# Kernel tuning notes

Hardware: AMD Instinct MI355X
Metric: run time of the kernel (lower is better)

## Reference

```python
import jax, jax.numpy as jnp
import numpy as np

N = 100000   # nodes
E = 600000   # edges
B = 512      # graphs in batch
H = 128      # hidden dim
ED = 8       # edge feature dim
TWO48 = float(2 ** 48 - 1)


def _w(k, shape, fan_in):
    return jax.random.normal(k, shape, jnp.float32) * (1.0 / np.sqrt(fan_in))


def setup_inputs() -> dict:
    key = jax.random.key(0)
    ks = jax.random.split(key, 32)
    inp = {}
    inp["s_node_ids"] = jax.random.randint(ks[0], (N,), 0, 2 ** 31 - 1, dtype=jnp.int32)
    inp["s_edge_index"] = jax.random.randint(ks[1], (2, E), 0, N, dtype=jnp.int32)
    inp["s_edge_attr"] = jax.random.normal(ks[2], (E, ED), jnp.float32)
    inp["s_batch"] = jnp.sort(jax.random.randint(ks[3], (N,), 0, B, dtype=jnp.int32))
    inp["depth"] = jax.random.uniform(ks[4], (B,), jnp.float32)
    # id_mlp: Linear(1,H) -> ReLU -> Linear(H,H)
    inp["id_w1"] = _w(ks[5], (1, H), 1); inp["id_b1"] = jnp.zeros((H,), jnp.float32)
    inp["id_w2"] = _w(ks[6], (H, H), H); inp["id_b2"] = jnp.zeros((H,), jnp.float32)
    # edge_mlp: Linear(ED,H) -> ReLU -> Linear(H,H)
    inp["ed_w1"] = _w(ks[7], (ED, H), ED); inp["ed_b1"] = jnp.zeros((H,), jnp.float32)
    inp["ed_w2"] = _w(ks[8], (H, H), H); inp["ed_b2"] = jnp.zeros((H,), jnp.float32)
    # GINEConv nn MLPs: Linear(H,H) -> ReLU -> Linear(H,H)
    inp["c1_w1"] = _w(ks[9], (H, H), H); inp["c1_b1"] = jnp.zeros((H,), jnp.float32)
    inp["c1_w2"] = _w(ks[10], (H, H), H); inp["c1_b2"] = jnp.zeros((H,), jnp.float32)
    inp["c2_w1"] = _w(ks[11], (H, H), H); inp["c2_b1"] = jnp.zeros((H,), jnp.float32)
    inp["c2_w2"] = _w(ks[12], (H, H), H); inp["c2_b2"] = jnp.zeros((H,), jnp.float32)
    inp["rg_w1"] = _w(ks[13], (H + 1, H), H + 1); inp["rg_b1"] = jnp.zeros((H,), jnp.float32)
    inp["rg_w2"] = _w(ks[14], (H, 1), H); inp["rg_b2"] = jnp.zeros((1,), jnp.float32)
    return inp


def _mlp2(x, w1, b1, w2, b2):
    return jax.nn.relu(x @ w1 + b1) @ w2 + b2


def _gine(x, src, dst, e, w1, b1, w2, b2):
    # message = ReLU(x_j + e), sum-aggregated at dst; out = nn((1+eps)*x + aggr), eps=0
    msg = jax.nn.relu(x[src] + e)                       # [E, H]
    aggr = jax.ops.segment_sum(msg, dst, num_segments=N)  # [N, H]
    return _mlp2(x + aggr, w1, b1, w2, b2)


def _global_mean(x, batch):
    sums = jax.ops.segment_sum(x, batch, num_segments=B)                          # [B, H]
    cnts = jax.ops.segment_sum(jnp.ones((x.shape[0], 1), x.dtype), batch, num_segments=B)
    return sums / jnp.maximum(cnts, 1.0)


def reference(s_node_ids, s_edge_index, s_edge_attr, s_batch, depth,
              id_w1, id_b1, id_w2, id_b2,
              ed_w1, ed_b1, ed_w2, ed_b2,
              c1_w1, c1_b1, c1_w2, c1_b2,
              c2_w1, c2_b1, c2_w2, c2_b2,
              rg_w1, rg_b1, rg_w2, rg_b2):
    src, dst = s_edge_index[0], s_edge_index[1]
    x0 = jnp.clip(s_node_ids.astype(jnp.float32) / TWO48, 0.0, 1.0)[:, None]  # [N,1]
    x = _mlp2(x0, id_w1, id_b1, id_w2, id_b2)                                 # [N,H]
    e = _mlp2(s_edge_attr, ed_w1, ed_b1, ed_w2, ed_b2)                        # [E,H]
    x = jax.nn.relu(_gine(x, src, dst, e, c1_w1, c1_b1, c1_w2, c1_b2))
    x = jax.nn.relu(_gine(x, src, dst, e, c2_w1, c2_b1, c2_w2, c2_b2))
    rep = jnp.concatenate([_global_mean(x, s_batch), depth[:, None]], axis=1)  # [B,H+1]
    return _mlp2(rep, rg_w1, rg_b1, rg_w2, rg_b2)[:, 0]                        # [B]
```

## Files before the change

### kernel.cpp

```cpp
#include <hip/hip_runtime.h>
#include <hip/hip_bf16.h>

#define N_NODES 100000
#define N_EDGES 600000
#define NB      512
#define H       128
#define ED      8
#define SCAN_CHUNK 1024
#define N_CHUNKS   98

typedef __attribute__((ext_vector_type(8))) short short8;
typedef __attribute__((ext_vector_type(4))) float f32x4;
typedef __attribute__((ext_vector_type(4))) unsigned int u32x4;
typedef unsigned short u16;
typedef unsigned int   u32;

static __device__ __forceinline__ u16 f2bf(float f) {
    u32 u = __float_as_uint(f);
    u32 r = u + 0x7fffu + ((u >> 16) & 1u);
    return (u16)(r >> 16);
}
static __device__ __forceinline__ float bf2f(u32 h) {
    return __uint_as_float(h << 16);
}

__global__ __launch_bounds__(256) void pack_all_kernel(
    const float* __restrict__ W0, const float* __restrict__ W1,
    const float* __restrict__ W2, const float* __restrict__ W3,
    const float* __restrict__ W4, const float* __restrict__ W5,
    const float* __restrict__ W6,
    short8* __restrict__ O0, short8* __restrict__ O1,
    short8* __restrict__ O2, short8* __restrict__ O3,
    short8* __restrict__ O4, short8* __restrict__ O5,
    short8* __restrict__ O6)
{
    int gid = blockIdx.x * 256 + threadIdx.x;
    const int total = 512 + 6 * 2048;
    if (gid >= total) return;
    const float* W; short8* O; int Krows, kkmax, slot;
    if (gid < 512) { W = W0; O = O0; Krows = ED; kkmax = 1; slot = gid; }
    else {
        int m = (gid - 512) / 2048;
        slot = (gid - 512) % 2048;
        Krows = H; kkmax = 4;
        switch (m) {
            case 0: W = W1; O = O1; break;
            case 1: W = W2; O = O2; break;
            case 2: W = W3; O = O3; break;
            case 3: W = W4; O = O4; break;
            case 4: W = W5; O = O5; break;
            default: W = W6; O = O6; break;
        }
    }
    int lane = slot & 63;
    int t = slot >> 6;
    int nt = t & 1; t >>= 1;
    int kk = t % kkmax;
    int w  = t / kkmax;
    int quad = lane >> 4, n15 = lane & 15;
    int n = w * 32 + nt * 16 + n15;
    short8 v;
    #pragma unroll
    for (int j = 0; j < 8; j++) {
        int k = kk * 32 + quad * 8 + j;
        v[j] = (k < Krows) ? (short)f2bf(W[k * H + n]) : (short)0;
    }
    O[slot] = v;
}

__global__ __launch_bounds__(256) void hist_kernel(
    const int* __restrict__ edge_index, int* __restrict__ counts)
{
    int e = blockIdx.x * 256 + threadIdx.x;
    if (e < N_EDGES) atomicAdd(&counts[edge_index[N_EDGES + e]], 1);
}

__global__ __launch_bounds__(SCAN_CHUNK) void scan1_kernel(
    const int* __restrict__ counts, int* __restrict__ chunk_scan,
    int* __restrict__ bsum_raw)
{
    __shared__ int s[SCAN_CHUNK];
    int tid = threadIdx.x;
    int gid = blockIdx.x * SCAN_CHUNK + tid;
    int v = counts[gid];
    s[tid] = v;
    __syncthreads();
    #pragma unroll
    for (int off = 1; off < SCAN_CHUNK; off <<= 1) {
        int t = (tid >= off) ? s[tid - off] : 0;
        __syncthreads();
        s[tid] += t;
        __syncthreads();
    }
    chunk_scan[gid] = s[tid] - v;
    if (tid == SCAN_CHUNK - 1) bsum_raw[blockIdx.x] = s[tid];
}

__global__ __launch_bounds__(128) void scan2_kernel(
    const int* __restrict__ bsum_raw, int* __restrict__ bsum_scan)
{
    __shared__ int s[128];
    int tid = threadIdx.x;
    int v = (tid < N_CHUNKS) ? bsum_raw[tid] : 0;
    s[tid] = v;
    __syncthreads();
    #pragma unroll
    for (int off = 1; off < 128; off <<= 1) {
        int t = (tid >= off) ? s[tid - off] : 0;
        __syncthreads();
        s[tid] += t;
        __syncthreads();
    }
    bsum_scan[tid] = s[tid] - v;
}

__global__ __launch_bounds__(256) void fill_kernel(
    const int* __restrict__ edge_index,
    const int* __restrict__ chunk_scan, const int* __restrict__ bsum_scan,
    int* __restrict__ counts, int* __restrict__ src_list,
    int* __restrict__ pos_of)
{
    int e = blockIdx.x * 256 + threadIdx.x;
    if (e >= N_EDGES) return;
    int src = edge_index[e];
    int dst = edge_index[N_EDGES + e];
    int slot = atomicAdd(&counts[dst], -1) - 1;
    int pos = chunk_scan[dst] + bsum_scan[dst >> 10] + slot;
    src_list[pos] = src;
    pos_of[e] = pos;
}

__global__ __launch_bounds__(256) void finalize_offsets(
    const int* __restrict__ chunk_scan, const int* __restrict__ bsum_scan,
    int* __restrict__ row_start)
{
    int i = blockIdx.x * 256 + threadIdx.x;
    if (i <= N_NODES) row_start[i] = chunk_scan[i] + bsum_scan[i >> 10];
}

__global__ __launch_bounds__(256) void node_mlp_mfma(
    const int* __restrict__ ids,
    const float* __restrict__ w1, const float* __restrict__ b1,
    const short8* __restrict__ pW2, const float* __restrict__ b2,
    u16* __restrict__ x_out)
{
    __shared__ u16 sH[64 * 136];
    __shared__ float s_x0[64];
    int tid = threadIdx.x;
    int w = tid >> 6, lane = tid & 63, quad = lane >> 4, n15 = lane & 15;
    short8 fW2[4][2];
    #pragma unroll
    for (int kk = 0; kk < 4; kk++) {
        fW2[kk][0] = pW2[((w * 4 + kk) * 2 + 0) * 64 + lane];
        fW2[kk][1] = pW2[((w * 4 + kk) * 2 + 1) * 64 + lane];
    }
    float rb2[2] = { b2[w * 32 + n15], b2[w * 32 + 16 + n15] };
    float w1c = w1[tid & 127], b1c = b1[tid & 127];
    const int ntile = (N_NODES + 63) / 64;
    for (int tile = blockIdx.x; tile < ntile; tile += gridDim.x) {
        int row0 = tile * 64;
        if (tid < 64) {
            int n = row0 + tid;
            float x0 = (n < N_NODES) ? (float)ids[n] / 281474976710655.0f : 0.0f;
            s_x0[tid] = fminf(fmaxf(x0, 0.0f), 1.0f);
        }
        __syncthreads();
        int half = tid >> 7, c = tid & 127;
        #pragma unroll 8
        for (int rr = 0; rr < 32; rr++) {
            int r = half + rr * 2;
            sH[r * 136 + c] = f2bf(fmaxf(s_x0[r] * w1c + b1c, 0.0f));
        }
        __syncthreads();
        f32x4 acc[4][2];
        #pragma unroll
        for (int s = 0; s < 4; s++) { acc[s][0] = (f32x4){0,0,0,0}; acc[s][1] = (f32x4){0,0,0,0}; }
        #pragma unroll
        for (int kk = 0; kk < 4; kk++) {
            #pragma unroll
            for (int s = 0; s < 4; s++) {
                short8 a = *(const short8*)&sH[(s * 16 + n15) * 136 + kk * 32 + quad * 8];
                acc[s][0] = __builtin_amdgcn_mfma_f32_16x16x32_bf16(a, fW2[kk][0], acc[s][0], 0, 0, 0);
                acc[s][1] = __builtin_amdgcn_mfma_f32_16x16x32_bf16(a, fW2[kk][1], acc[s][1], 0, 0, 0);
            }
        }
        __syncthreads();
        #pragma unroll
        for (int s = 0; s < 4; s++)
            #pragma unroll
            for (int nt = 0; nt < 2; nt++) {
                int col = w * 32 + nt * 16 + n15;
                #pragma unroll
                for (int reg = 0; reg < 4; reg++)
                    sH[(s * 16 + quad * 4 + reg) * 136 + col] =
                        f2bf(acc[s][nt][reg] + rb2[nt]);
            }
        __syncthreads();
        for (int idx = tid; idx < 64 * 16; idx += 256) {
            int r = idx >> 4, c8 = (idx & 15) << 3;
            int n = row0 + r;
            if (n < N_NODES)
                *(uint4*)&x_out[(long)n * H + c8] = *(const uint4*)&sH[r * 136 + c8];
        }
        __syncthreads();
    }
}

__global__ __launch_bounds__(256) void edge_mlp_mfma(
    const float* __restrict__ attr,
    const int* __restrict__ pos_of,
    const short8* __restrict__ pW1, const float* __restrict__ b1,
    const short8* __restrict__ pW2, const float* __restrict__ b2,
    u16* __restrict__ e_perm)
{
    __shared__ u16 sA[64 * 40];
    __shared__ u16 sH[64 * 136];
    __shared__ int sPos[64];
    int tid = threadIdx.x;
    int w = tid >> 6, lane = tid & 63, quad = lane >> 4, n15 = lane & 15;
    short8 fW1[2];
    fW1[0] = pW1[(w * 2 + 0) * 64 + lane];
    fW1[1] = pW1[(w * 2 + 1) * 64 + lane];
    short8 fW2[4][2];
    #pragma unroll
    for (int kk = 0; kk < 4; kk++) {
        fW2[kk][0] = pW2[((w * 4 + kk) * 2 + 0) * 64 + lane];
        fW2[kk][1] = pW2[((w * 4 + kk) * 2 + 1) * 64 + lane];
    }
    float rb1[2] = { b1[w * 32 + n15], b1[w * 32 + 16 + n15] };
    float rb2[2] = { b2[w * 32 + n15], b2[w * 32 + 16 + n15] };
    const int ntile = N_EDGES / 64;
    for (int tile = blockIdx.x; tile < ntile; tile += gridDim.x) {
        int row0 = tile * 64;
        if (tid < 64) sPos[tid] = pos_of[row0 + tid];
        if (tid >= 64 && tid < 192) {
            int t2 = tid - 64;
            int r = t2 >> 1, c4 = (t2 & 1) * 4;
            f32x4 v = __builtin_nontemporal_load((const f32x4*)&attr[(long)(row0 + r) * ED + c4]);
            ushort4 o;
            o.x = f2bf(v[0]); o.y = f2bf(v[1]); o.z = f2bf(v[2]); o.w = f2bf(v[3]);
            *(ushort4*)&sA[r * 40 + c4] = o;
        } else if (tid >= 192) {
            int idx = tid - 192;
            for (; idx < 192; idx += 64) {
                int r = idx / 3, c8 = 8 + (idx % 3) * 8;
                *(uint4*)&sA[r * 40 + c8] = make_uint4(0, 0, 0, 0);
            }
        }
        __syncthreads();
        f32x4 acc[4][2];
        #pragma unroll
        for (int s = 0; s < 4; s++) { acc[s][0] = (f32x4){0,0,0,0}; acc[s][1] = (f32x4){0,0,0,0}; }
        #pragma unroll
        for (int s = 0; s < 4; s++) {
            short8 a = *(const short8*)&sA[(s * 16 + n15) * 40 + quad * 8];
            acc[s][0] = __builtin_amdgcn_mfma_f32_16x16x32_bf16(a, fW1[0], acc[s][0], 0, 0, 0);
            acc[s][1] = __builtin_amdgcn_mfma_f32_16x16x32_bf16(a, fW1[1], acc[s][1], 0, 0, 0);
        }
        #pragma unroll
        for (int s = 0; s < 4; s++)
            #pragma unroll
            for (int nt = 0; nt < 2; nt++) {
                int col = w * 32 + nt * 16 + n15;
                #pragma unroll
                for (int reg = 0; reg < 4; reg++)
                    sH[(s * 16 + quad * 4 + reg) * 136 + col] =
                        f2bf(fmaxf(acc[s][nt][reg] + rb1[nt], 0.0f));
            }
        __syncthreads();
        #pragma unroll
        for (int s = 0; s < 4; s++) { acc[s][0] = (f32x4){0,0,0,0}; acc[s][1] = (f32x4){0,0,0,0}; }
        #pragma unroll
        for (int kk = 0; kk < 4; kk++) {
            #pragma unroll
            for (int s = 0; s < 4; s++) {
                short8 a = *(const short8*)&sH[(s * 16 + n15) * 136 + kk * 32 + quad * 8];
                acc[s][0] = __builtin_amdgcn_mfma_f32_16x16x32_bf16(a, fW2[kk][0], acc[s][0], 0, 0, 0);
                acc[s][1] = __builtin_amdgcn_mfma_f32_16x16x32_bf16(a, fW2[kk][1], acc[s][1], 0, 0, 0);
            }
        }
        __syncthreads();
        #pragma unroll
        for (int s = 0; s < 4; s++)
            #pragma unroll
            for (int nt = 0; nt < 2; nt++) {
                int col = w * 32 + nt * 16 + n15;
                #pragma unroll
                for (int reg = 0; reg < 4; reg++)
                    sH[(s * 16 + quad * 4 + reg) * 136 + col] =
                        f2bf(acc[s][nt][reg] + rb2[nt]);
            }
        __syncthreads();
        for (int idx = tid; idx < 64 * 16; idx += 256) {
            int r = idx >> 4, c8 = (idx & 15) << 3;
            long rr = sPos[r];
            u32x4 v = *(const u32x4*)&sH[r * 136 + c8];
            __builtin_nontemporal_store(v, (u32x4*)&e_perm[rr * H + c8]);
        }
        __syncthreads();
    }
}

static __device__ __forceinline__ void acc8(float* a, u32x4 xv, u32x4 ev) {
    #pragma unroll
    for (int q = 0; q < 4; q++) {
        a[2 * q + 0] += fmaxf(bf2f(xv[q] & 0xffff) + bf2f(ev[q] & 0xffff), 0.0f);
        a[2 * q + 1] += fmaxf(bf2f(xv[q] >> 16)    + bf2f(ev[q] >> 16),    0.0f);
    }
}

__global__ __launch_bounds__(256) void aggregate_kernel(
    const int* __restrict__ row_start,
    const int* __restrict__ src_list,
    const u16* __restrict__ e_perm,
    const u16* __restrict__ x,
    u16* __restrict__ xs_out)
{
    int tid  = threadIdx.x;
    int lane = tid & 63;
    int l16  = lane & 15;
    int base = lane & 48;
    int fo   = l16 * 8;
    int n = blockIdx.x * 16 + (tid >> 4);
    const u16* xb = x + fo;

    int beg = row_start[n];
    int end = row_start[n + 1];
    float a[8], b[8];
    #pragma unroll
    for (int q = 0; q < 8; q++) { a[q] = 0.0f; b[q] = 0.0f; }

    for (int j0 = beg; j0 < end; j0 += 16) {
        int m = min(16, end - j0);
        int sv = src_list[j0 + min(l16, m - 1)];
        const u16* ej = e_perm + (long)j0 * H + fo;
        int j = 0;
        for (; j + 2 <= m; j += 2) {
            int s0 = __shfl(sv, base | j);
            int s1 = __shfl(sv, base | (j + 1));
            u32x4 xv0 = *(const u32x4*)(xb + (long)s0 * H);
            u32x4 ev0 = __builtin_nontemporal_load((const u32x4*)(ej + (long)(j + 0) * H));
            u32x4 xv1 = *(const u32x4*)(xb + (long)s1 * H);
            u32x4 ev1 = __builtin_nontemporal_load((const u32x4*)(ej + (long)(j + 1) * H));
            acc8(a, xv0, ev0);
            acc8(b, xv1, ev1);
        }
        if (j < m) {
            int s0 = __shfl(sv, base | j);
            u32x4 xv0 = *(const u32x4*)(xb + (long)s0 * H);
            u32x4 ev0 = __builtin_nontemporal_load((const u32x4*)(ej + (long)j * H));
            acc8(a, xv0, ev0);
        }
    }
    u32x4 xself = *(const u32x4*)(xb + (long)n * H);
    u32x4 out;
    #pragma unroll
    for (int q = 0; q < 4; q++) {
        float o0 = bf2f(xself[q] & 0xffff) + a[2 * q + 0] + b[2 * q + 0];
        float o1 = bf2f(xself[q] >> 16)    + a[2 * q + 1] + b[2 * q + 1];
        out[q] = (u32)f2bf(o0) | ((u32)f2bf(o1) << 16);
    }
    __builtin_nontemporal_store(out, (u32x4*)&xs_out[(long)n * H + fo]);
}

__global__ __launch_bounds__(256) void conv_mlp_mfma(
    const u16* __restrict__ xs,
    const short8* __restrict__ pW1, const float* __restrict__ b1,
    const short8* __restrict__ pW2, const float* __restrict__ b2,
    u16* __restrict__ x_out)
{
    __shared__ u16 sA[32 * 136];
    int tid = threadIdx.x;
    int w = tid >> 6, lane = tid & 63, quad = lane >> 4, n15 = lane & 15;
    short8 fW1[4][2], fW2[4][2];
    #pragma unroll
    for (int kk = 0; kk < 4; kk++) {
        fW1[kk][0] = pW1[((w * 4 + kk) * 2 + 0) * 64 + lane];
        fW1[kk][1] = pW1[((w * 4 + kk) * 2 + 1) * 64 + lane];
        fW2[kk][0] = pW2[((w * 4 + kk) * 2 + 0) * 64 + lane];
        fW2[kk][1] = pW2[((w * 4 + kk) * 2 + 1) * 64 + lane];
    }
    float rb1[2] = { b1[w * 32 + n15], b1[w * 32 + 16 + n15] };
    float rb2[2] = { b2[w * 32 + n15], b2[w * 32 + 16 + n15] };
    const int ntile = N_NODES / 32;
    for (int tile = blockIdx.x; tile < ntile; tile += gridDim.x) {
        long row0 = (long)tile * 32;
        for (int idx = tid; idx < 32 * 16; idx += 256) {
            int r = idx >> 4, c8 = (idx & 15) << 3;
            *(uint4*)&sA[r * 136 + c8] = *(const uint4*)&xs[(row0 + r) * H + c8];
        }
        __syncthreads();
        f32x4 acc[2][2];
        #pragma unroll
        for (int s = 0; s < 2; s++) { acc[s][0] = (f32x4){0,0,0,0}; acc[s][1] = (f32x4){0,0,0,0}; }
        #pragma unroll
        for (int kk = 0; kk < 4; kk++) {
            #pragma unroll
            for (int s = 0; s < 2; s++) {
                short8 a = *(const short8*)&sA[(s * 16 + n15) * 136 + kk * 32 + quad * 8];
                acc[s][0] = __builtin_amdgcn_mfma_f32_16x16x32_bf16(a, fW1[kk][0], acc[s][0], 0, 0, 0);
                acc[s][1] = __builtin_amdgcn_mfma_f32_16x16x32_bf16(a, fW1[kk][1], acc[s][1], 0, 0, 0);
            }
        }
        __syncthreads();
        #pragma unroll
        for (int s = 0; s < 2; s++)
            #pragma unroll
            for (int nt = 0; nt < 2; nt++) {
                int col = w * 32 + nt * 16 + n15;
                #pragma unroll
                for (int reg = 0; reg < 4; reg++)
                    sA[(s * 16 + quad * 4 + reg) * 136 + col] =
                        f2bf(fmaxf(acc[s][nt][reg] + rb1[nt], 0.0f));
            }
        __syncthreads();
        #pragma unroll
        for (int s = 0; s < 2; s++) { acc[s][0] = (f32x4){0,0,0,0}; acc[s][1] = (f32x4){0,0,0,0}; }
        #pragma unroll
        for (int kk = 0; kk < 4; kk++) {
            #pragma unroll
            for (int s = 0; s < 2; s++) {
                short8 a = *(const short8*)&sA[(s * 16 + n15) * 136 + kk * 32 + quad * 8];
                acc[s][0] = __builtin_amdgcn_mfma_f32_16x16x32_bf16(a, fW2[kk][0], acc[s][0], 0, 0, 0);
                acc[s][1] = __builtin_amdgcn_mfma_f32_16x16x32_bf16(a, fW2[kk][1], acc[s][1], 0, 0, 0);
            }
        }
        __syncthreads();
        #pragma unroll
        for (int s = 0; s < 2; s++)
            #pragma unroll
            for (int nt = 0; nt < 2; nt++) {
                int col = w * 32 + nt * 16 + n15;
                #pragma unroll
                for (int reg = 0; reg < 4; reg++)
                    sA[(s * 16 + quad * 4 + reg) * 136 + col] =
                        f2bf(fmaxf(acc[s][nt][reg] + rb2[nt], 0.0f));
            }
        __syncthreads();
        for (int idx = tid; idx < 32 * 16; idx += 256) {
            int r = idx >> 4, c8 = (idx & 15) << 3;
            *(uint4*)&x_out[(row0 + r) * H + c8] = *(const uint4*)&sA[r * 136 + c8];
        }
        __syncthreads();
    }
}

__global__ __launch_bounds__(256) void pool_kernel(
    const u16* __restrict__ x, const int* __restrict__ batch,
    float* __restrict__ sums, float* __restrict__ cnt)
{
    int sg   = threadIdx.x >> 6;
    int lane = threadIdx.x & 63;
    int fo = lane * 2;
    const int nper = (N_NODES + gridDim.x - 1) / gridDim.x;
    int n0 = blockIdx.x * nper;
    int n1 = min(n0 + nper, N_NODES);
    int cur = -1;
    float a0 = 0.0f, a1 = 0.0f, c = 0.0f;
    for (int n = n0 + sg; n < n1; n += 4) {
        int b = batch[n];
        if (b != cur) {
            if (cur >= 0) {
                atomicAdd(&sums[cur * H + fo],     a0);
                atomicAdd(&sums[cur * H + fo + 1], a1);
                if (lane == 0) atomicAdd(&cnt[cur], c);
            }
            a0 = a1 = 0.0f; c = 0.0f; cur = b;
        }
        u32 xv = *(const u32*)&x[(long)n * H + fo];
        a0 += bf2f(xv & 0xffff);
        a1 += bf2f(xv >> 16);
        c += 1.0f;
    }
    if (cur >= 0) {
        atomicAdd(&sums[cur * H + fo],     a0);
        atomicAdd(&sums[cur * H + fo + 1], a1);
        if (lane == 0) atomicAdd(&cnt[cur], c);
    }
}

__global__ __launch_bounds__(128) void regressor_kernel(
    const float* __restrict__ sums, const float* __restrict__ cnt,
    const float* __restrict__ depth,
    const float* __restrict__ w1, const float* __restrict__ b1,
    const float* __restrict__ w2, const float* __restrict__ b2,
    float* __restrict__ out)
{
    __shared__ float s_mean[H];
    __shared__ float s_red[2];
    int b = blockIdx.x;
    int j = threadIdx.x;
    float c = fmaxf(cnt[b], 1.0f);
    s_mean[j] = sums[b * H + j] / c;
    __syncthreads();
    float h = b1[j];
    #pragma unroll 8
    for (int k = 0; k < H; k++) h += s_mean[k] * w1[k * H + j];
    h += depth[b] * w1[H * H + j];
    h = fmaxf(h, 0.0f);
    float p = h * w2[j];
    #pragma unroll
    for (int off = 32; off >= 1; off >>= 1) p += __shfl_down(p, off, 64);
    if ((j & 63) == 0) s_red[j >> 6] = p;
    __syncthreads();
    if (j == 0) out[b] = s_red[0] + s_red[1] + b2[0];
}

extern "C" void kernel_launch(void* const* d_in, const int* in_sizes, int n_in,
                              void* d_out, int out_size, void* d_ws, size_t ws_size,
                              hipStream_t stream)
{
    const int*   ids   = (const int*)  d_in[0];
    const int*   eidx  = (const int*)  d_in[1];
    const float* eattr = (const float*)d_in[2];
    const int*   batch = (const int*)  d_in[3];
    const float* depth = (const float*)d_in[4];
    const float* id_w1 = (const float*)d_in[5];
    const float* id_b1 = (const float*)d_in[6];
    const float* id_w2 = (const float*)d_in[7];
    const float* id_b2 = (const float*)d_in[8];
    const float* ed_w1 = (const float*)d_in[9];
    const float* ed_b1 = (const float*)d_in[10];
    const float* ed_w2 = (const float*)d_in[11];
    const float* ed_b2 = (const float*)d_in[12];
    const float* c1_w1 = (const float*)d_in[13];
    const float* c1_b1 = (const float*)d_in[14];
    const float* c1_w2 = (const float*)d_in[15];
    const float* c1_b2 = (const float*)d_in[16];
    const float* c2_w1 = (const float*)d_in[17];
    const float* c2_b1 = (const float*)d_in[18];
    const float* c2_w2 = (const float*)d_in[19];
    const float* c2_b2 = (const float*)d_in[20];
    const float* rg_w1 = (const float*)d_in[21];
    const float* rg_b1 = (const float*)d_in[22];
    const float* rg_w2 = (const float*)d_in[23];
    const float* rg_b2 = (const float*)d_in[24];

    char* ws = (char*)d_ws;
    u16*   e_buf    = (u16*)  (ws);
    u16*   x_buf    = (u16*)  (ws + 153600000);
    u16*   xs_buf   = (u16*)  (ws + 179200000);
    float* sums_buf = (float*)(ws + 204800000);
    float* cnt_buf  = (float*)(ws + 205062144);
    int*   counts   = (int*)  (ws + 205064192);
    int*   chunk_sc = (int*)  (ws + 205465600);
    int*   bsum_raw = (int*)  (ws + 205867008);
    int*   bsum_sc  = (int*)  (ws + 205867520);
    int*   src_list = (int*)  (ws + 205868032);
    int*   pos_of   = (int*)  (ws + 208268032);
    short8* ed_w1p  = (short8*)(ws + 210668032);
    short8* ed_w2p  = (short8*)(ws + 210676224);
    short8* c1_w1p  = (short8*)(ws + 210708992);
    short8* c1_w2p  = (short8*)(ws + 210741760);
    short8* c2_w1p  = (short8*)(ws + 210774528);
    short8* c2_w2p  = (short8*)(ws + 210807296);
    short8* id_w2p  = (short8*)(ws + 210840064);
    int*   row_start = counts;

    pack_all_kernel<<<50, 256, 0, stream>>>(
        ed_w1, ed_w2, c1_w1, c1_w2, c2_w1, c2_w2, id_w2,
        ed_w1p, ed_w2p, c1_w1p, c1_w2p, c2_w1p, c2_w2p, id_w2p);

    hipMemsetAsync(counts, 0, 401408, stream);
    hist_kernel <<<(N_EDGES + 255) / 256, 256, 0, stream>>>(eidx, counts);
    scan1_kernel<<<N_CHUNKS, SCAN_CHUNK, 0, stream>>>(counts, chunk_sc, bsum_raw);
    scan2_kernel<<<1, 128, 0, stream>>>(bsum_raw, bsum_sc);
    fill_kernel <<<(N_EDGES + 255) / 256, 256, 0, stream>>>(eidx, chunk_sc, bsum_sc,
                                                            counts, src_list, pos_of);
    finalize_offsets<<<(N_NODES + 256) / 256, 256, 0, stream>>>(chunk_sc, bsum_sc, row_start);

    node_mlp_mfma<<<768, 256, 0, stream>>>(ids, id_w1, id_b1, id_w2p, id_b2, x_buf);
    edge_mlp_mfma<<<2048, 256, 0, stream>>>(eattr, pos_of, ed_w1p, ed_b1, ed_w2p, ed_b2, e_buf);

    aggregate_kernel<<<6250, 256, 0, stream>>>(row_start, src_list, e_buf, x_buf, xs_buf);
    conv_mlp_mfma<<<3125, 256, 0, stream>>>(xs_buf, c1_w1p, c1_b1, c1_w2p, c1_b2, x_buf);

    aggregate_kernel<<<6250, 256, 0, stream>>>(row_start, src_list, e_buf, x_buf, xs_buf);
    conv_mlp_mfma<<<3125, 256, 0, stream>>>(xs_buf, c2_w1p, c2_b1, c2_w2p, c2_b2, x_buf);

    hipMemsetAsync(sums_buf, 0, (size_t)(NB * H + NB) * 4, stream);
    pool_kernel<<<2048, 256, 0, stream>>>(x_buf, batch, sums_buf, cnt_buf);
    regressor_kernel<<<NB, 128, 0, stream>>>(sums_buf, cnt_buf, depth,
                                             rg_w1, rg_b1, rg_w2, rg_b2, (float*)d_out);
}
```

Measured before the change: 408.1 us.

## Permute edge attributes in fill, pack bf16 pairs, aggregate two nodes per group

The fill kernel now converts edge attributes to bf16 and scatters them into CSR order. The edge MLP can then read its inputs directly into registers and write the edge embeddings contiguously, with no pos_of indirection, no scattered stores and no LDS staging of the input. Bf16 rounding now uses the packed v_cvt_pk_bf16_f32 instruction across all MLP epilogues. The aggregate kernel handles two destination nodes per 16-lane group with interleaved loads to raise memory-level parallelism, at the cost of more registers, more complex control flow and half as many blocks.

```diff
diff --git a/kernel.cpp b/kernel.cpp
--- a/kernel.cpp
+++ b/kernel.cpp
@@ -22,6 +22,11 @@
 }
 static __device__ __forceinline__ float bf2f(u32 h) {
     return __uint_as_float(h << 16);
+}
+static __device__ __forceinline__ u32 bfpack(float lo, float hi) {
+    u32 r;
+    asm("v_cvt_pk_bf16_f32 %0, %1, %2" : "=v"(r) : "v"(lo), "v"(hi));
+    return r;
 }
 
 __global__ __launch_bounds__(256) void pack_all_kernel(
@@ -118,7 +123,7 @@
     const int* __restrict__ edge_index,
     const int* __restrict__ chunk_scan, const int* __restrict__ bsum_scan,
     int* __restrict__ counts, int* __restrict__ src_list,
-    int* __restrict__ pos_of)
+    const float* __restrict__ attr, u16* __restrict__ attr_perm)
 {
     int e = blockIdx.x * 256 + threadIdx.x;
     if (e >= N_EDGES) return;
@@ -127,7 +132,13 @@
     int slot = atomicAdd(&counts[dst], -1) - 1;
     int pos = chunk_scan[dst] + bsum_scan[dst >> 10] + slot;
     src_list[pos] = src;
-    pos_of[e] = pos;
+    float4 v0 = *(const float4*)&attr[(long)e * ED];
+    float4 v1 = *(const float4*)&attr[(long)e * ED + 4];
+    u32 w0 = bfpack(v0.x, v0.y);
+    u32 w1 = bfpack(v0.z, v0.w);
+    u32 w2 = bfpack(v1.x, v1.y);
+    u32 w3 = bfpack(v1.z, v1.w);
+    *(uint4*)&attr_perm[(long)pos * ED] = make_uint4(w0, w1, w2, w3);
 }
 
 __global__ __launch_bounds__(256) void finalize_offsets(
@@ -166,10 +177,13 @@
         }
         __syncthreads();
         int half = tid >> 7, c = tid & 127;
-        #pragma unroll 8
-        for (int rr = 0; rr < 32; rr++) {
+        #pragma unroll
+        for (int rr = 0; rr < 32; rr += 2) {
             int r = half + rr * 2;
-            sH[r * 136 + c] = f2bf(fmaxf(s_x0[r] * w1c + b1c, 0.0f));
+            u32 p = bfpack(fmaxf(s_x0[r] * w1c + b1c, 0.0f),
+                           fmaxf(s_x0[r + 2] * w1c + b1c, 0.0f));
+            sH[r * 136 + c]       = (u16)p;
+            sH[(r + 2) * 136 + c] = (u16)(p >> 16);
         }
         __syncthreads();
         f32x4 acc[4][2];
@@ -190,10 +204,13 @@
             #pragma unroll
             for (int nt = 0; nt < 2; nt++) {
                 int col = w * 32 + nt * 16 + n15;
-                #pragma unroll
-                for (int reg = 0; reg < 4; reg++)
-                    sH[(s * 16 + quad * 4 + reg) * 136 + col] =
-                        f2bf(acc[s][nt][reg] + rb2[nt]);
+                int rb = (s * 16 + quad * 4) * 136 + col;
+                u32 p0 = bfpack(acc[s][nt][0] + rb2[nt], acc[s][nt][1] + rb2[nt]);
+                u32 p1 = bfpack(acc[s][nt][2] + rb2[nt], acc[s][nt][3] + rb2[nt]);
+                sH[rb]       = (u16)p0;
+                sH[rb + 136] = (u16)(p0 >> 16);
+                sH[rb + 272] = (u16)p1;
+                sH[rb + 408] = (u16)(p1 >> 16);
             }
         __syncthreads();
         for (int idx = tid; idx < 64 * 16; idx += 256) {
@@ -207,15 +224,12 @@
 }
 
 __global__ __launch_bounds__(256) void edge_mlp_mfma(
-    const float* __restrict__ attr,
-    const int* __restrict__ pos_of,
+    const u16* __restrict__ attr_perm,
     const short8* __restrict__ pW1, const float* __restrict__ b1,
     const short8* __restrict__ pW2, const float* __restrict__ b2,
     u16* __restrict__ e_perm)
 {
-    __shared__ u16 sA[64 * 40];
     __shared__ u16 sH[64 * 136];
-    __shared__ int sPos[64];
     int tid = threadIdx.x;
     int w = tid >> 6, lane = tid & 63, quad = lane >> 4, n15 = lane & 15;
     short8 fW1[2];
@@ -229,43 +243,39 @@
     }
     float rb1[2] = { b1[w * 32 + n15], b1[w * 32 + 16 + n15] };
     float rb2[2] = { b2[w * 32 + n15], b2[w * 32 + 16 + n15] };
+    const short8 zero8 = (short8){0,0,0,0,0,0,0,0};
     const int ntile = N_EDGES / 64;
     for (int tile = blockIdx.x; tile < ntile; tile += gridDim.x) {
         int row0 = tile * 64;
-        if (tid < 64) sPos[tid] = pos_of[row0 + tid];
-        if (tid >= 64 && tid < 192) {
-            int t2 = tid - 64;
-            int r = t2 >> 1, c4 = (t2 & 1) * 4;
-            f32x4 v = __builtin_nontemporal_load((const f32x4*)&attr[(long)(row0 + r) * ED + c4]);
-            ushort4 o;
-            o.x = f2bf(v[0]); o.y = f2bf(v[1]); o.z = f2bf(v[2]); o.w = f2bf(v[3]);
-            *(ushort4*)&sA[r * 40 + c4] = o;
-        } else if (tid >= 192) {
-            int idx = tid - 192;
-            for (; idx < 192; idx += 64) {
-                int r = idx / 3, c8 = 8 + (idx % 3) * 8;
-                *(uint4*)&sA[r * 40 + c8] = make_uint4(0, 0, 0, 0);
-            }
-        }
-        __syncthreads();
+        short8 av[4];
+        #pragma unroll
+        for (int s = 0; s < 4; s++) {
+            av[s] = zero8;
+            if (quad == 0)
+                av[s] = *(const short8*)&attr_perm[(long)(row0 + s * 16 + n15) * ED];
+        }
         f32x4 acc[4][2];
         #pragma unroll
         for (int s = 0; s < 4; s++) { acc[s][0] = (f32x4){0,0,0,0}; acc[s][1] = (f32x4){0,0,0,0}; }
         #pragma unroll
         for (int s = 0; s < 4; s++) {
-            short8 a = *(const short8*)&sA[(s * 16 + n15) * 40 + quad * 8];
-            acc[s][0] = __builtin_amdgcn_mfma_f32_16x16x32_bf16(a, fW1[0], acc[s][0], 0, 0, 0);
-            acc[s][1] = __builtin_amdgcn_mfma_f32_16x16x32_bf16(a, fW1[1], acc[s][1], 0, 0, 0);
+            acc[s][0] = __builtin_amdgcn_mfma_f32_16x16x32_bf16(av[s], fW1[0], acc[s][0], 0, 0, 0);
+            acc[s][1] = __builtin_amdgcn_mfma_f32_16x16x32_bf16(av[s], fW1[1], acc[s][1], 0, 0, 0);
         }
         #pragma unroll
         for (int s = 0; s < 4; s++)
             #pragma unroll
             for (int nt = 0; nt < 2; nt++) {
                 int col = w * 32 + nt * 16 + n15;
-                #pragma unroll
-                for (int reg = 0; reg < 4; reg++)
-                    sH[(s * 16 + quad * 4 + reg) * 136 + col] =
-                        f2bf(fmaxf(acc[s][nt][reg] + rb1[nt], 0.0f));
+                int rb = (s * 16 + quad * 4) * 136 + col;
+                u32 p0 = bfpack(fmaxf(acc[s][nt][0] + rb1[nt], 0.0f),
+                                fmaxf(acc[s][nt][1] + rb1[nt], 0.0f));
+                u32 p1 = bfpack(fmaxf(acc[s][nt][2] + rb1[nt], 0.0f),
+                                fmaxf(acc[s][nt][3] + rb1[nt], 0.0f));
+                sH[rb]       = (u16)p0;
+                sH[rb + 136] = (u16)(p0 >> 16);
+                sH[rb + 272] = (u16)p1;
+                sH[rb + 408] = (u16)(p1 >> 16);
             }
         __syncthreads();
         #pragma unroll
@@ -285,17 +295,18 @@
             #pragma unroll
             for (int nt = 0; nt < 2; nt++) {
                 int col = w * 32 + nt * 16 + n15;
-                #pragma unroll
-                for (int reg = 0; reg < 4; reg++)
-                    sH[(s * 16 + quad * 4 + reg) * 136 + col] =
-                        f2bf(acc[s][nt][reg] + rb2[nt]);
+                int rb = (s * 16 + quad * 4) * 136 + col;
+                u32 p0 = bfpack(acc[s][nt][0] + rb2[nt], acc[s][nt][1] + rb2[nt]);
+                u32 p1 = bfpack(acc[s][nt][2] + rb2[nt], acc[s][nt][3] + rb2[nt]);
+                sH[rb]       = (u16)p0;
+                sH[rb + 136] = (u16)(p0 >> 16);
+                sH[rb + 272] = (u16)p1;
+                sH[rb + 408] = (u16)(p1 >> 16);
             }
         __syncthreads();
         for (int idx = tid; idx < 64 * 16; idx += 256) {
             int r = idx >> 4, c8 = (idx & 15) << 3;
-            long rr = sPos[r];
-            u32x4 v = *(const u32x4*)&sH[r * 136 + c8];
-            __builtin_nontemporal_store(v, (u32x4*)&e_perm[rr * H + c8]);
+            *(uint4*)&e_perm[(long)(row0 + r) * H + c8] = *(const uint4*)&sH[r * 136 + c8];
         }
         __syncthreads();
     }
@@ -321,46 +332,111 @@
     int l16  = lane & 15;
     int base = lane & 48;
     int fo   = l16 * 8;
-    int n = blockIdx.x * 16 + (tid >> 4);
+    int g    = tid >> 4;
+    int nA   = blockIdx.x * 32 + g * 2;
     const u16* xb = x + fo;
 
-    int beg = row_start[n];
-    int end = row_start[n + 1];
-    float a[8], b[8];
-    #pragma unroll
-    for (int q = 0; q < 8; q++) { a[q] = 0.0f; b[q] = 0.0f; }
-
-    for (int j0 = beg; j0 < end; j0 += 16) {
-        int m = min(16, end - j0);
-        int sv = src_list[j0 + min(l16, m - 1)];
-        const u16* ej = e_perm + (long)j0 * H + fo;
-        int j = 0;
-        for (; j + 2 <= m; j += 2) {
-            int s0 = __shfl(sv, base | j);
-            int s1 = __shfl(sv, base | (j + 1));
-            u32x4 xv0 = *(const u32x4*)(xb + (long)s0 * H);
-            u32x4 ev0 = __builtin_nontemporal_load((const u32x4*)(ej + (long)(j + 0) * H));
-            u32x4 xv1 = *(const u32x4*)(xb + (long)s1 * H);
-            u32x4 ev1 = __builtin_nontemporal_load((const u32x4*)(ej + (long)(j + 1) * H));
-            acc8(a, xv0, ev0);
-            acc8(b, xv1, ev1);
-        }
-        if (j < m) {
-            int s0 = __shfl(sv, base | j);
-            u32x4 xv0 = *(const u32x4*)(xb + (long)s0 * H);
-            u32x4 ev0 = __builtin_nontemporal_load((const u32x4*)(ej + (long)j * H));
-            acc8(a, xv0, ev0);
-        }
-    }
-    u32x4 xself = *(const u32x4*)(xb + (long)n * H);
-    u32x4 out;
+    int rsA = row_start[nA];
+    int rsB = row_start[nA + 1];
+    int rsC = row_start[nA + 2];
+    float a0[8], a1[8], b0[8], b1[8];
+    #pragma unroll
+    for (int q = 0; q < 8; q++) { a0[q] = 0.0f; a1[q] = 0.0f; b0[q] = 0.0f; b1[q] = 0.0f; }
+
+    int jA = rsA, endA = rsB;
+    int jB = rsB, endB = rsC;
+    while (jA < endA || jB < endB) {
+        int mA = endA - jA; mA = mA > 16 ? 16 : (mA < 0 ? 0 : mA);
+        int mB = endB - jB; mB = mB > 16 ? 16 : (mB < 0 ? 0 : mB);
+        int svA = mA ? src_list[jA + min(l16, mA - 1)] : 0;
+        int svB = mB ? src_list[jB + min(l16, mB - 1)] : 0;
+        const u16* eA = e_perm + (long)jA * H + fo;
+        const u16* eB = e_perm + (long)jB * H + fo;
+        int mD = mA < mB ? mA : mB;
+        int i = 0;
+        for (; i + 2 <= mD; i += 2) {
+            int sa0 = __shfl(svA, base | i);
+            int sa1 = __shfl(svA, base | (i + 1));
+            int sb0 = __shfl(svB, base | i);
+            int sb1 = __shfl(svB, base | (i + 1));
+            u32x4 va0 = *(const u32x4*)(xb + (long)sa0 * H);
+            u32x4 wa0 = *(const u32x4*)(eA + (long)(i + 0) * H);
+            u32x4 vb0 = *(const u32x4*)(xb + (long)sb0 * H);
+            u32x4 wb0 = *(const u32x4*)(eB + (long)(i + 0) * H);
+            u32x4 va1 = *(const u32x4*)(xb + (long)sa1 * H);
+            u32x4 wa1 = *(const u32x4*)(eA + (long)(i + 1) * H);
+            u32x4 vb1 = *(const u32x4*)(xb + (long)sb1 * H);
+            u32x4 wb1 = *(const u32x4*)(eB + (long)(i + 1) * H);
+            acc8(a0, va0, wa0);
+            acc8(b0, vb0, wb0);
+            acc8(a1, va1, wa1);
+            acc8(b1, vb1, wb1);
+        }
+        if (i < mD) {
+            int sa0 = __shfl(svA, base | i);
+            int sb0 = __shfl(svB, base | i);
+            u32x4 va0 = *(const u32x4*)(xb + (long)sa0 * H);
+            u32x4 wa0 = *(const u32x4*)(eA + (long)i * H);
+            u32x4 vb0 = *(const u32x4*)(xb + (long)sb0 * H);
+            u32x4 wb0 = *(const u32x4*)(eB + (long)i * H);
+            acc8(a0, va0, wa0);
+            acc8(b0, vb0, wb0);
+            i++;
+        }
+        int k = i;
+        for (; k + 2 <= mA; k += 2) {
+            int sa0 = __shfl(svA, base | k);
+            int sa1 = __shfl(svA, base | (k + 1));
+            u32x4 va0 = *(const u32x4*)(xb + (long)sa0 * H);
+            u32x4 wa0 = *(const u32x4*)(eA + (long)(k + 0) * H);
+            u32x4 va1 = *(const u32x4*)(xb + (long)sa1 * H);
+            u32x4 wa1 = *(const u32x4*)(eA + (long)(k + 1) * H);
+            acc8(a0, va0, wa0);
+            acc8(a1, va1, wa1);
+        }
+        if (k < mA) {
+            int sa0 = __shfl(svA, base | k);
+            u32x4 va0 = *(const u32x4*)(xb + (long)sa0 * H);
+            u32x4 wa0 = *(const u32x4*)(eA + (long)k * H);
+            acc8(a0, va0, wa0);
+        }
+        k = i;
+        for (; k + 2 <= mB; k += 2) {
+            int sb0 = __shfl(svB, base | k);
+            int sb1 = __shfl(svB, base | (k + 1));
+            u32x4 vb0 = *(const u32x4*)(xb + (long)sb0 * H);
+            u32x4 wb0 = *(const u32x4*)(eB + (long)(k + 0) * H);
+            u32x4 vb1 = *(const u32x4*)(xb + (long)sb1 * H);
+            u32x4 wb1 = *(const u32x4*)(eB + (long)(k + 1) * H);
+            acc8(b0, vb0, wb0);
+            acc8(b1, vb1, wb1);
+        }
+        if (k < mB) {
+            int sb0 = __shfl(svB, base | k);
+            u32x4 vb0 = *(const u32x4*)(xb + (long)sb0 * H);
+            u32x4 wb0 = *(const u32x4*)(eB + (long)k * H);
+            acc8(b0, vb0, wb0);
+        }
+        jA += mA; jB += mB;
+    }
+    u32x4 xvA = *(const u32x4*)(xb + (long)nA * H);
+    u32x4 oA;
     #pragma unroll
     for (int q = 0; q < 4; q++) {
-        float o0 = bf2f(xself[q] & 0xffff) + a[2 * q + 0] + b[2 * q + 0];
-        float o1 = bf2f(xself[q] >> 16)    + a[2 * q + 1] + b[2 * q + 1];
-        out[q] = (u32)f2bf(o0) | ((u32)f2bf(o1) << 16);
-    }
-    __builtin_nontemporal_store(out, (u32x4*)&xs_out[(long)n * H + fo]);
+        float o0 = bf2f(xvA[q] & 0xffff) + (a0[2 * q + 0] + a1[2 * q + 0]);
+        float o1 = bf2f(xvA[q] >> 16)    + (a0[2 * q + 1] + a1[2 * q + 1]);
+        oA[q] = bfpack(o0, o1);
+    }
+    *(u32x4*)&xs_out[(long)nA * H + fo] = oA;
+    u32x4 xvB = *(const u32x4*)(xb + (long)(nA + 1) * H);
+    u32x4 oB;
+    #pragma unroll
+    for (int q = 0; q < 4; q++) {
+        float o0 = bf2f(xvB[q] & 0xffff) + (b0[2 * q + 0] + b1[2 * q + 0]);
+        float o1 = bf2f(xvB[q] >> 16)    + (b0[2 * q + 1] + b1[2 * q + 1]);
+        oB[q] = bfpack(o0, o1);
+    }
+    *(u32x4*)&xs_out[(long)(nA + 1) * H + fo] = oB;
 }
 
 __global__ __launch_bounds__(256) void conv_mlp_mfma(
@@ -408,10 +484,15 @@
             #pragma unroll
             for (int nt = 0; nt < 2; nt++) {
                 int col = w * 32 + nt * 16 + n15;
-                #pragma unroll
-                for (int reg = 0; reg < 4; reg++)
-                    sA[(s * 16 + quad * 4 + reg) * 136 + col] =
-                        f2bf(fmaxf(acc[s][nt][reg] + rb1[nt], 0.0f));
+                int rb = (s * 16 + quad * 4) * 136 + col;
+                u32 p0 = bfpack(fmaxf(acc[s][nt][0] + rb1[nt], 0.0f),
+                                fmaxf(acc[s][nt][1] + rb1[nt], 0.0f));
+                u32 p1 = bfpack(fmaxf(acc[s][nt][2] + rb1[nt], 0.0f),
+                                fmaxf(acc[s][nt][3] + rb1[nt], 0.0f));
+                sA[rb]       = (u16)p0;
+                sA[rb + 136] = (u16)(p0 >> 16);
+                sA[rb + 272] = (u16)p1;
+                sA[rb + 408] = (u16)(p1 >> 16);
             }
         __syncthreads();
         #pragma unroll
@@ -431,10 +512,15 @@
             #pragma unroll
             for (int nt = 0; nt < 2; nt++) {
                 int col = w * 32 + nt * 16 + n15;
-                #pragma unroll
-                for (int reg = 0; reg < 4; reg++)
-                    sA[(s * 16 + quad * 4 + reg) * 136 + col] =
-                        f2bf(fmaxf(acc[s][nt][reg] + rb2[nt], 0.0f));
+                int rb = (s * 16 + quad * 4) * 136 + col;
+                u32 p0 = bfpack(fmaxf(acc[s][nt][0] + rb2[nt], 0.0f),
+                                fmaxf(acc[s][nt][1] + rb2[nt], 0.0f));
+                u32 p1 = bfpack(fmaxf(acc[s][nt][2] + rb2[nt], 0.0f),
+                                fmaxf(acc[s][nt][3] + rb2[nt], 0.0f));
+                sA[rb]       = (u16)p0;
+                sA[rb + 136] = (u16)(p0 >> 16);
+                sA[rb + 272] = (u16)p1;
+                sA[rb + 408] = (u16)(p1 >> 16);
             }
         __syncthreads();
         for (int idx = tid; idx < 32 * 16; idx += 256) {
@@ -547,15 +633,15 @@
     int*   bsum_raw = (int*)  (ws + 205867008);
     int*   bsum_sc  = (int*)  (ws + 205867520);
     int*   src_list = (int*)  (ws + 205868032);
-    int*   pos_of   = (int*)  (ws + 208268032);
-    short8* ed_w1p  = (short8*)(ws + 210668032);
-    short8* ed_w2p  = (short8*)(ws + 210676224);
-    short8* c1_w1p  = (short8*)(ws + 210708992);
-    short8* c1_w2p  = (short8*)(ws + 210741760);
-    short8* c2_w1p  = (short8*)(ws + 210774528);
-    short8* c2_w2p  = (short8*)(ws + 210807296);
-    short8* id_w2p  = (short8*)(ws + 210840064);
+    short8* ed_w1p  = (short8*)(ws + 208268032);
+    short8* ed_w2p  = (short8*)(ws + 208276224);
+    short8* c1_w1p  = (short8*)(ws + 208308992);
+    short8* c1_w2p  = (short8*)(ws + 208341760);
+    short8* c2_w1p  = (short8*)(ws + 208374528);
+    short8* c2_w2p  = (short8*)(ws + 208407296);
+    short8* id_w2p  = (short8*)(ws + 208440064);
     int*   row_start = counts;
+    u16*   attr_perm = xs_buf;
 
     pack_all_kernel<<<50, 256, 0, stream>>>(
         ed_w1, ed_w2, c1_w1, c1_w2, c2_w1, c2_w2, id_w2,
@@ -566,16 +652,17 @@
     scan1_kernel<<<N_CHUNKS, SCAN_CHUNK, 0, stream>>>(counts, chunk_sc, bsum_raw);
     scan2_kernel<<<1, 128, 0, stream>>>(bsum_raw, bsum_sc);
     fill_kernel <<<(N_EDGES + 255) / 256, 256, 0, stream>>>(eidx, chunk_sc, bsum_sc,
-                                                            counts, src_list, pos_of);
+                                                            counts, src_list,
+                                                            eattr, attr_perm);
     finalize_offsets<<<(N_NODES + 256) / 256, 256, 0, stream>>>(chunk_sc, bsum_sc, row_start);
 
     node_mlp_mfma<<<768, 256, 0, stream>>>(ids, id_w1, id_b1, id_w2p, id_b2, x_buf);
-    edge_mlp_mfma<<<2048, 256, 0, stream>>>(eattr, pos_of, ed_w1p, ed_b1, ed_w2p, ed_b2, e_buf);
-
-    aggregate_kernel<<<6250, 256, 0, stream>>>(row_start, src_list, e_buf, x_buf, xs_buf);
+    edge_mlp_mfma<<<2048, 256, 0, stream>>>(attr_perm, ed_w1p, ed_b1, ed_w2p, ed_b2, e_buf);
+
+    aggregate_kernel<<<3125, 256, 0, stream>>>(row_start, src_list, e_buf, x_buf, xs_buf);
     conv_mlp_mfma<<<3125, 256, 0, stream>>>(xs_buf, c1_w1p, c1_b1, c1_w2p, c1_b2, x_buf);
 
-    aggregate_kernel<<<6250, 256, 0, stream>>>(row_start, src_list, e_buf, x_buf, xs_buf);
+    aggregate_kernel<<<3125, 256, 0, stream>>>(row_start, src_list, e_buf, x_buf, xs_buf);
     conv_mlp_mfma<<<3125, 256, 0, stream>>>(xs_buf, c2_w1p, c2_b1, c2_w2p, c2_b2, x_buf);
 
     hipMemsetAsync(sums_buf, 0, (size_t)(NB * H + NB) * 4, stream);
```

Result: slower. 425.8 us (+4.3%).
